# Kernel optimization log

Measured on AMD Instinct MI355X. Metric: run time of the kernel, lower is better.

The kernel has to match this reference:

```python
import jax, jax.numpy as jnp
import numpy as np
import math

B, S, HID = 2, 2048, 2048
NH, NKV, HD = 32, 8, 64
THETA = 10000.0
EPS = 1e-6
LAYER_IDX = 1
LAMBDA_INIT = 0.8 - 0.6 * math.exp(-0.3 * LAYER_IDX)
LAMBDA_STD = 0.1


def setup_inputs() -> dict:
    key = jax.random.key(0)
    ks = jax.random.split(key, 10)
    hidden_states = jax.random.normal(ks[0], (B, S, HID), jnp.float32)
    # RoPE cos/sin, llama convention: emb = cat(freqs, freqs)
    inv_freq = 1.0 / (THETA ** (np.arange(0, HD, 2, dtype=np.float32) / HD))
    freqs = np.outer(np.arange(S, dtype=np.float32), inv_freq)  # [S, HD/2]
    emb = np.concatenate([freqs, freqs], axis=-1)                # [S, HD]
    cos = jnp.broadcast_to(jnp.asarray(np.cos(emb), jnp.float32)[None], (B, S, HD))
    sin = jnp.broadcast_to(jnp.asarray(np.sin(emb), jnp.float32)[None], (B, S, HD))
    # additive causal mask [B,1,S,S]
    causal = jnp.triu(jnp.full((S, S), -1e9, dtype=jnp.float32), k=1)
    attention_mask = jnp.broadcast_to(causal[None, None], (B, 1, S, S))
    sc = 0.02
    wq = sc * jax.random.normal(ks[1], (NH * HD, HID), jnp.float32)
    wk = sc * jax.random.normal(ks[2], (NKV * HD, HID), jnp.float32)
    wv = sc * jax.random.normal(ks[3], (NKV * HD, HID), jnp.float32)
    wo = sc * jax.random.normal(ks[4], (HID, NH * HD), jnp.float32)
    lambda_q1 = LAMBDA_STD * jax.random.normal(ks[5], (HD,), jnp.float32)
    lambda_k1 = LAMBDA_STD * jax.random.normal(ks[6], (HD,), jnp.float32)
    lambda_q2 = LAMBDA_STD * jax.random.normal(ks[7], (HD,), jnp.float32)
    lambda_k2 = LAMBDA_STD * jax.random.normal(ks[8], (HD,), jnp.float32)
    return {"hidden_states": hidden_states, "cos": cos, "sin": sin,
            "attention_mask": attention_mask, "wq": wq, "wk": wk, "wv": wv,
            "wo": wo, "lambda_q1": lambda_q1, "lambda_k1": lambda_k1,
            "lambda_q2": lambda_q2, "lambda_k2": lambda_k2}


def _rotate_half(x):
    x1, x2 = jnp.split(x, 2, axis=-1)
    return jnp.concatenate([-x2, x1], axis=-1)


def reference(hidden_states, cos, sin, attention_mask, wq, wk, wv, wo,
              lambda_q1, lambda_k1, lambda_q2, lambda_k2):
    b, s, _ = hidden_states.shape
    # projections -> [b, h, s, d]
    q = jnp.einsum('bsh,oh->bso', hidden_states, wq).reshape(b, s, NH, HD).transpose(0, 2, 1, 3)
    k = jnp.einsum('bsh,oh->bso', hidden_states, wk).reshape(b, s, NKV, HD).transpose(0, 2, 1, 3)
    v = jnp.einsum('bsh,oh->bso', hidden_states, wv).reshape(b, s, NKV, HD).transpose(0, 2, 1, 3)
    # rotary
    c, sn = cos[:, None], sin[:, None]  # [b,1,s,d]
    q = q * c + _rotate_half(q) * sn
    k = k * c + _rotate_half(k) * sn
    # GQA repeat
    groups = NH // NKV
    k = jnp.repeat(k, groups, axis=1)
    v = jnp.repeat(v, groups, axis=1)
    # diff-attention value trick: pair head i with head i+NH/2 -> [b, NH, s, 2d]
    v = jnp.concatenate([v[:, :NH // 2], v[:, NH // 2:]], axis=-1)  # [b, NH/2, s, 2d]
    v = jnp.concatenate([v, v], axis=1)                              # [b, NH, s, 2d]
    # scores + causal mask, stable softmax in fp32
    aw = jnp.einsum('bhqd,bhkd->bhqk', q, k) / math.sqrt(HD)
    aw = aw + attention_mask
    aw = jax.nn.softmax(aw.astype(jnp.float32), axis=-1).astype(q.dtype)
    ao = jnp.einsum('bhqk,bhkd->bhqd', aw, v)  # [b, NH, s, 2d]
    lam1 = jnp.exp(jnp.sum((lambda_q1 * lambda_k1).astype(jnp.float32)))
    lam2 = jnp.exp(jnp.sum((lambda_q2 * lambda_k2).astype(jnp.float32)))
    lam = (lam1 - lam2).astype(q.dtype) + LAMBDA_INIT
    a1, a2 = ao[:, :NH // 2], ao[:, NH // 2:]
    out = a1 - lam * a2  # [b, NH/2, s, 2d]
    # RMSNorm over last dim (no affine)
    out = out * jax.lax.rsqrt(jnp.mean(out * out, axis=-1, keepdims=True) + EPS)
    out = (1.0 - LAMBDA_INIT) * out
    out = out.transpose(0, 2, 1, 3).reshape(b, s, NH * HD)
    return jnp.einsum('bso,ho->bsh', out, wo)
```

## Files before the change

### kernel.cpp

```cpp
#include <hip/hip_runtime.h>

typedef __attribute__((ext_vector_type(8))) short bhalf8;
typedef __attribute__((ext_vector_type(4))) float floatx4;

constexpr int B_ = 2, S_ = 2048, HID_ = 2048, NH_ = 32, NKV_ = 8, HD_ = 64;
constexpr float LAMBDA_INIT_F = 0.35550906759096924f;
constexpr float EPS_ = 1e-6f;
constexpr float QSCALE_ = 0.18033688011112042f;

#define DEVINL __device__ __forceinline__

DEVINL float bf2f(unsigned short u) {
    union { unsigned u; float f; } v; v.u = ((unsigned)u) << 16; return v.f;
}
DEVINL unsigned short f2bf(float f) {
    union { float f; unsigned u; } v; v.f = f;
    unsigned u = v.u;
    return (unsigned short)((u + 0x7fffu + ((u >> 16) & 1u)) >> 16);
}
DEVINL float fexp2(float x) {
#if __has_builtin(__builtin_amdgcn_exp2f)
    return __builtin_amdgcn_exp2f(x);
#else
    return exp2f(x);
#endif
}
DEVINL unsigned pk_bf16(float a, float b) {
#if __has_builtin(__builtin_amdgcn_cvt_pk_bf16_f32)
    typedef __bf16 bf16x2_t __attribute__((ext_vector_type(2)));
    bf16x2_t p = __builtin_amdgcn_cvt_pk_bf16_f32(a, b);
    unsigned r;
    __builtin_memcpy(&r, &p, 4);
    return r;
#else
    return (unsigned)f2bf(a) | ((unsigned)f2bf(b) << 16);
#endif
}
DEVINL void load_lds16(const unsigned short* g, unsigned short* l) {
    __builtin_amdgcn_global_load_lds(
        (const __attribute__((address_space(1))) unsigned int*)g,
        (__attribute__((address_space(3))) unsigned int*)l, 16, 0, 0);
}

__global__ __launch_bounds__(256)
void cvt_all(const float* __restrict__ hs, const float* __restrict__ wq,
             const float* __restrict__ wk, const float* __restrict__ wv,
             const float* __restrict__ wo, unsigned short* __restrict__ hs_bf,
             unsigned short* __restrict__ wcat, unsigned short* __restrict__ wo_bf) {
    const size_t i = (size_t)(blockIdx.x * 256 + threadIdx.x) * 4;
    const float* src;
    unsigned short* dst;
    size_t off;
    float scale = 1.f;
    if (i < 8388608) { src = hs; dst = hs_bf; off = 0; }
    else if (i < 12582912) { src = wq; dst = wcat; off = 8388608; scale = QSCALE_; }
    else if (i < 13631488) { src = wk; dst = wcat + 4194304; off = 12582912; }
    else if (i < 14680064) { src = wv; dst = wcat + 5242880; off = 13631488; }
    else { src = wo; dst = wo_bf; off = 14680064; }
    const size_t k = i - off;
    const float4 v = *(const float4*)(src + k);
    ushort4 o;
    o.x = f2bf(v.x * scale); o.y = f2bf(v.y * scale);
    o.z = f2bf(v.z * scale); o.w = f2bf(v.w * scale);
    *(ushort4*)(dst + k) = o;
}

__global__ void lam_kernel(const float* __restrict__ q1, const float* __restrict__ k1,
                           const float* __restrict__ q2, const float* __restrict__ k2,
                           float* __restrict__ lam) {
    const int l = threadIdx.x;
    float p1 = q1[l] * k1[l];
    float p2 = q2[l] * k2[l];
    #pragma unroll
    for (int off = 1; off < 64; off <<= 1) {
        p1 += __shfl_xor(p1, off, 64);
        p2 += __shfl_xor(p2, off, 64);
    }
    if (l == 0) *lam = expf(p1) - expf(p2) + LAMBDA_INIT_F;
}

__global__ __launch_bounds__(256)
void gemm_qkv(const unsigned short* __restrict__ A, const unsigned short* __restrict__ Bw,
              const float* __restrict__ cosb, const float* __restrict__ sinb,
              unsigned short* __restrict__ Qr, unsigned short* __restrict__ Kr,
              unsigned short* __restrict__ VT) {
    constexpr int K = 2048;
    union GS {
        struct { unsigned short A[2][128][32]; unsigned short B[2][128][32]; } d;
        unsigned short vt[128][130];
    };
    __shared__ __align__(16) GS gsm;
    const int t = threadIdx.x;
    const int w = t >> 6, lane = t & 63, quad = lane >> 4, lid = lane & 15;
    const int wr = (w >> 1) * 64, wc = (w & 1) * 64;
    const long bm = (long)blockIdx.x * 128, bn = (long)blockIdx.y * 128;

    floatx4 acc[4][4];
    #pragma unroll
    for (int i = 0; i < 4; i++)
        #pragma unroll
        for (int j = 0; j < 4; j++) acc[i][j] = (floatx4){0.f, 0.f, 0.f, 0.f};

    const int s0 = t, s1 = t + 256;
    const unsigned short* Ag0 = A + (bm + (s0 >> 2)) * (long)K + (s0 & 3) * 8;
    const unsigned short* Ag1 = A + (bm + (s1 >> 2)) * (long)K + (s1 & 3) * 8;
    const unsigned short* Bg0 = Bw + (bn + (s0 >> 2)) * (long)K + (s0 & 3) * 8;
    const unsigned short* Bg1 = Bw + (bn + (s1 >> 2)) * (long)K + (s1 & 3) * 8;
    const int l0 = s0 * 8, l1 = s1 * 8;

    load_lds16(Ag0, &gsm.d.A[0][0][0] + l0);
    load_lds16(Ag1, &gsm.d.A[0][0][0] + l1);
    load_lds16(Bg0, &gsm.d.B[0][0][0] + l0);
    load_lds16(Bg1, &gsm.d.B[0][0][0] + l1);
    __syncthreads();

    const int nk = K >> 5;
    for (int kt = 0; kt < nk; kt++) {
        const int cur = kt & 1, nxt = cur ^ 1;
        if (kt + 1 < nk) {
            const int off = (kt + 1) << 5;
            load_lds16(Ag0 + off, &gsm.d.A[nxt][0][0] + l0);
            load_lds16(Ag1 + off, &gsm.d.A[nxt][0][0] + l1);
            load_lds16(Bg0 + off, &gsm.d.B[nxt][0][0] + l0);
            load_lds16(Bg1 + off, &gsm.d.B[nxt][0][0] + l1);
        }
        bhalf8 af[4], bf[4];
        #pragma unroll
        for (int i = 0; i < 4; i++) af[i] = *(const bhalf8*)&gsm.d.A[cur][wr + i * 16 + lid][quad * 8];
        #pragma unroll
        for (int j = 0; j < 4; j++) bf[j] = *(const bhalf8*)&gsm.d.B[cur][wc + j * 16 + lid][quad * 8];
        #pragma unroll
        for (int i = 0; i < 4; i++)
            #pragma unroll
            for (int j = 0; j < 4; j++)
                acc[i][j] = __builtin_amdgcn_mfma_f32_16x16x32_bf16(af[i], bf[j], acc[i][j], 0, 0, 0);
        __syncthreads();
    }

    const int y = blockIdx.y;
    if (y < 20) {
        const bool isQ = (y < 16);
        #pragma unroll
        for (int i = 0; i < 4; i++) {
            #pragma unroll
            for (int r = 0; r < 4; r++) {
                const long row = bm + wr + i * 16 + quad * 4 + r;
                const int bb = (int)(row >> 11), s = (int)(row & 2047);
                const float* cp = cosb + (size_t)row * 64;
                const float* sp = sinb + (size_t)row * 64;
                #pragma unroll
                for (int jj = 0; jj < 4; jj++) {
                    const int col = (int)bn + wc + jj * 16 + lid;
                    const int d = col & 63;
                    const float x = acc[i][jj][r];
                    const float oth = acc[i][jj ^ 2][r];
                    const float rot = (jj < 2) ? -oth : oth;
                    const float yv = x * cp[d] + rot * sp[d];
                    if (isQ) {
                        const int h = col >> 6;
                        Qr[((size_t)(bb * NH_ + h) * S_ + s) * HD_ + d] = f2bf(yv);
                    } else {
                        const int h = (col - 2048) >> 6;
                        Kr[((size_t)(bb * NKV_ + h) * S_ + s) * HD_ + d] = f2bf(yv);
                    }
                }
            }
        }
    } else {
        #pragma unroll
        for (int i = 0; i < 4; i++)
            #pragma unroll
            for (int jj = 0; jj < 4; jj++)
                #pragma unroll
                for (int r = 0; r < 4; r++)
                    gsm.vt[wr + i * 16 + quad * 4 + r][wc + jj * 16 + lid] = f2bf(acc[i][jj][r]);
        __syncthreads();
        const int b0 = (int)(bm >> 11), sbase = (int)(bm & 2047);
        #pragma unroll 4
        for (int it = 0; it < 32; it++) {
            const int d = w + 4 * it;
            const int colg = (int)bn + d;
            const int h = (colg - 2560) >> 6;
            const int dl = colg & 63;
            const int sl = lane * 2;
            const unsigned v = (unsigned)gsm.vt[sl][d] | ((unsigned)gsm.vt[sl + 1][d] << 16);
            *(unsigned*)(VT + ((size_t)(b0 * NKV_ + h) * HD_ + dl) * S_ + sbase + sl) = v;
        }
    }
}

__global__ __launch_bounds__(256)
void gemm_bt(const unsigned short* __restrict__ A, const unsigned short* __restrict__ Bw,
             float* __restrict__ Cout, int M, int N, int K) {
    __shared__ __align__(16) unsigned short As[2][128][32];
    __shared__ __align__(16) unsigned short Bs[2][128][32];
    const int t = threadIdx.x;
    const int w = t >> 6, lane = t & 63, quad = lane >> 4, lid = lane & 15;
    const int wr = (w >> 1) * 64, wc = (w & 1) * 64;
    const long bm = (long)blockIdx.x * 128, bn = (long)blockIdx.y * 128;

    floatx4 acc[4][4];
    #pragma unroll
    for (int i = 0; i < 4; i++)
        #pragma unroll
        for (int j = 0; j < 4; j++) acc[i][j] = (floatx4){0.f, 0.f, 0.f, 0.f};

    const int s0 = t, s1 = t + 256;
    const unsigned short* Ag0 = A + (bm + (s0 >> 2)) * (long)K + (s0 & 3) * 8;
    const unsigned short* Ag1 = A + (bm + (s1 >> 2)) * (long)K + (s1 & 3) * 8;
    const unsigned short* Bg0 = Bw + (bn + (s0 >> 2)) * (long)K + (s0 & 3) * 8;
    const unsigned short* Bg1 = Bw + (bn + (s1 >> 2)) * (long)K + (s1 & 3) * 8;
    const int l0 = s0 * 8, l1 = s1 * 8;

    load_lds16(Ag0, &As[0][0][0] + l0);
    load_lds16(Ag1, &As[0][0][0] + l1);
    load_lds16(Bg0, &Bs[0][0][0] + l0);
    load_lds16(Bg1, &Bs[0][0][0] + l1);
    __syncthreads();

    const int nk = K >> 5;
    for (int kt = 0; kt < nk; kt++) {
        const int cur = kt & 1, nxt = cur ^ 1;
        if (kt + 1 < nk) {
            const int off = (kt + 1) << 5;
            load_lds16(Ag0 + off, &As[nxt][0][0] + l0);
            load_lds16(Ag1 + off, &As[nxt][0][0] + l1);
            load_lds16(Bg0 + off, &Bs[nxt][0][0] + l0);
            load_lds16(Bg1 + off, &Bs[nxt][0][0] + l1);
        }
        bhalf8 af[4], bf[4];
        #pragma unroll
        for (int i = 0; i < 4; i++) af[i] = *(const bhalf8*)&As[cur][wr + i * 16 + lid][quad * 8];
        #pragma unroll
        for (int j = 0; j < 4; j++) bf[j] = *(const bhalf8*)&Bs[cur][wc + j * 16 + lid][quad * 8];
        #pragma unroll
        for (int i = 0; i < 4; i++)
            #pragma unroll
            for (int j = 0; j < 4; j++)
                acc[i][j] = __builtin_amdgcn_mfma_f32_16x16x32_bf16(af[i], bf[j], acc[i][j], 0, 0, 0);
        __syncthreads();
    }

    #pragma unroll
    for (int i = 0; i < 4; i++) {
        #pragma unroll
        for (int j = 0; j < 4; j++) {
            const long row = bm + wr + i * 16 + quad * 4;
            const long col = bn + wc + j * 16 + lid;
            #pragma unroll
            for (int r = 0; r < 4; r++) Cout[(row + r) * N + col] = acc[i][j][r];
        }
    }
}

__global__ __launch_bounds__(512, 4)
void attn_diff(const unsigned short* __restrict__ Qr, const unsigned short* __restrict__ Kr,
               const unsigned short* __restrict__ VT, const float* __restrict__ lamp,
               unsigned short* __restrict__ attn) {
    union SM {
        struct {
            unsigned short Kt[2][64][72];
            unsigned short Vt[128][72];
            unsigned short Pt[8][16][72];
        } a;
        unsigned short Ot[2][64][136];
    };
    __shared__ __align__(16) SM sm;

    const int j = blockIdx.y, b = blockIdx.z;
    const int t = threadIdx.x;
    const int w = t >> 6, lane = t & 63, quad = lane >> 4, lid = lane & 15;
    const int st = w >> 2;
    const int rh = (w & 3) * 16;
    const int kv1 = j >> 2, kv2 = 4 + (j >> 2);
    const int qhead = j + st * 16;
    const float lam = *lamp;

    const int ss = t >> 8, kidx = t & 255;
    const int key_s = kidx >> 2, dh = (kidx & 3) * 16;
    const unsigned short* ksrc0 = Kr + (size_t)(b * NKV_ + (ss ? kv2 : kv1)) * S_ * HD_ +
                                  (size_t)key_s * HD_ + dh;
    const int d7 = t >> 2, vh = (t & 3) * 16;
    const unsigned short* vsrc0 = VT + ((size_t)(b * NKV_ + (d7 < 64 ? kv1 : kv2)) * HD_ +
                                        (d7 & 63)) * (size_t)S_ + vh;

    for (int half = 0; half < 2; half++) {
        const int qt = half ? (31 - (int)blockIdx.x) : (int)blockIdx.x;
        const int qb = qt * 64;

        const unsigned short* qbase =
            Qr + ((size_t)((b * NH_ + qhead) * S_) + qb + rh + lid) * HD_;
        const bhalf8 qa0 = *(const bhalf8*)(qbase + quad * 8);
        const bhalf8 qa1 = *(const bhalf8*)(qbase + 32 + quad * 8);

        floatx4 acc[8];
        #pragma unroll
        for (int c = 0; c < 8; c++) acc[c] = (floatx4){0.f, 0.f, 0.f, 0.f};
        float l_acc[4] = {0.f, 0.f, 0.f, 0.f};

        const int nkt = qt + 1;

        for (int kt = 0; kt < nkt; kt++) {
            const int k0 = kt * 64;
            const unsigned short* kp = ksrc0 + (size_t)k0 * HD_;
            const unsigned short* vp = vsrc0 + k0;
            int4 kr0 = *(const int4*)(kp);
            int4 kr1 = *(const int4*)(kp + 8);
            int4 vr0 = *(const int4*)(vp);
            int4 vr1 = *(const int4*)(vp + 8);
            __syncthreads();
            *(int4*)&sm.a.Kt[ss][key_s][dh] = kr0;
            *(int4*)&sm.a.Kt[ss][key_s][dh + 8] = kr1;
            *(int4*)&sm.a.Vt[d7][vh] = vr0;
            *(int4*)&sm.a.Vt[d7][vh + 8] = vr1;
            __syncthreads();

            const bool last = (kt == nkt - 1);
            const int nt_lim = last ? ((w & 3) + 1) : 4;

            floatx4 sc[4];
            #pragma unroll
            for (int nt = 0; nt < 4; nt++) {
                if (nt < nt_lim) {
                    const bhalf8 kb0 = *(const bhalf8*)&sm.a.Kt[st][nt * 16 + lid][quad * 8];
                    const bhalf8 kb1 = *(const bhalf8*)&sm.a.Kt[st][nt * 16 + lid][32 + quad * 8];
                    floatx4 z = (floatx4){0.f, 0.f, 0.f, 0.f};
                    z = __builtin_amdgcn_mfma_f32_16x16x32_bf16(qa0, kb0, z, 0, 0, 0);
                    z = __builtin_amdgcn_mfma_f32_16x16x32_bf16(qa1, kb1, z, 0, 0, 0);
                    sc[nt] = z;
                }
            }

            if (last) {
                #pragma unroll
                for (int nt = 0; nt < 4; nt++) {
                    const int keyg = k0 + nt * 16 + lid;
                    #pragma unroll
                    for (int r = 0; r < 4; r++) {
                        float p = 0.f;
                        if (nt < nt_lim) {
                            const int rowg = qb + rh + quad * 4 + r;
                            p = (keyg > rowg) ? 0.f : fexp2(sc[nt][r]);
                        }
                        sc[nt][r] = p;
                        l_acc[r] += p;
                    }
                }
            } else {
                #pragma unroll
                for (int nt = 0; nt < 4; nt++)
                    #pragma unroll
                    for (int r = 0; r < 4; r++) {
                        const float p = fexp2(sc[nt][r]);
                        sc[nt][r] = p;
                        l_acc[r] += p;
                    }
            }

            #pragma unroll
            for (int nt = 0; nt < 4; nt++) {
                #pragma unroll
                for (int r = 0; r < 4; r += 2) {
                    const unsigned pk = pk_bf16(sc[nt][r], sc[nt][r + 1]);
                    sm.a.Pt[w][quad * 4 + r][nt * 16 + lid] = (unsigned short)(pk & 0xffff);
                    sm.a.Pt[w][quad * 4 + r + 1][nt * 16 + lid] = (unsigned short)(pk >> 16);
                }
            }

            #pragma unroll
            for (int kk = 0; kk < 2; kk++) {
                if (nt_lim > kk * 2) {
                    const bhalf8 pa = *(const bhalf8*)&sm.a.Pt[w][lid][kk * 32 + quad * 8];
                    #pragma unroll
                    for (int c = 0; c < 8; c++) {
                        const bhalf8 vb = *(const bhalf8*)&sm.a.Vt[c * 16 + lid][kk * 32 + quad * 8];
                        acc[c] = __builtin_amdgcn_mfma_f32_16x16x32_bf16(pa, vb, acc[c], 0, 0, 0);
                    }
                }
            }
        }

        #pragma unroll
        for (int off = 1; off < 16; off <<= 1)
            #pragma unroll
            for (int r = 0; r < 4; r++) l_acc[r] += __shfl_xor(l_acc[r], off, 64);

        __syncthreads();
        #pragma unroll
        for (int r = 0; r < 4; r++) {
            const float rl = 1.0f / l_acc[r];
            #pragma unroll
            for (int c = 0; c < 8; c++)
                sm.Ot[st][rh + quad * 4 + r][c * 16 + lid] = f2bf(acc[c][r] * rl);
        }
        __syncthreads();

        const int row = t >> 3, m = t & 7;
        float vals[16];
        float ssum = 0.f;
        #pragma unroll
        for (int c = 0; c < 4; c++) {
            const unsigned long long u0 = *(const unsigned long long*)&sm.Ot[0][row][m * 4 + 32 * c];
            const unsigned long long u1 = *(const unsigned long long*)&sm.Ot[1][row][m * 4 + 32 * c];
            #pragma unroll
            for (int i = 0; i < 4; i++) {
                const float x = bf2f((unsigned short)(u0 >> (16 * i))) -
                                lam * bf2f((unsigned short)(u1 >> (16 * i)));
                vals[c * 4 + i] = x;
                ssum += x * x;
            }
        }
        ssum += __shfl_xor(ssum, 1, 64);
        ssum += __shfl_xor(ssum, 2, 64);
        ssum += __shfl_xor(ssum, 4, 64);
        const float scale = (1.f - LAMBDA_INIT_F) * rsqrtf(ssum * (1.f / 128.f) + EPS_);
        unsigned short* dst = attn + (size_t)(b * S_ + qb + row) * (NH_ * HD_) + j * 128 + m * 4;
        #pragma unroll
        for (int c = 0; c < 4; c++) {
            unsigned short ob[4];
            #pragma unroll
            for (int i = 0; i < 4; i++) ob[i] = f2bf(vals[c * 4 + i] * scale);
            *(unsigned long long*)(dst + 32 * c) = *(const unsigned long long*)ob;
        }
        __syncthreads();
    }
}

extern "C" void kernel_launch(void* const* d_in, const int* in_sizes, int n_in,
                              void* d_out, int out_size, void* d_ws, size_t ws_size,
                              hipStream_t stream) {
    const float* hs   = (const float*)d_in[0];
    const float* cosb = (const float*)d_in[1];
    const float* sinb = (const float*)d_in[2];
    const float* wq   = (const float*)d_in[4];
    const float* wk   = (const float*)d_in[5];
    const float* wv   = (const float*)d_in[6];
    const float* wo   = (const float*)d_in[7];
    const float* lq1  = (const float*)d_in[8];
    const float* lk1  = (const float*)d_in[9];
    const float* lq2  = (const float*)d_in[10];
    const float* lk2  = (const float*)d_in[11];

    unsigned short* p = (unsigned short*)d_ws;
    unsigned short* hs_bf = p;  p += (size_t)4096 * 2048;
    unsigned short* wcat  = p;  p += (size_t)3072 * 2048;
    unsigned short* wo_bf = p;  p += (size_t)2048 * 2048;
    unsigned short* Qr    = p;  p += (size_t)B_ * NH_ * S_ * HD_;
    unsigned short* Kr    = p;  p += (size_t)B_ * NKV_ * S_ * HD_;
    unsigned short* VT    = p;  p += (size_t)B_ * NKV_ * S_ * HD_;
    unsigned short* attnb = p;  p += (size_t)4096 * 2048;
    float* lam = (float*)p;

    cvt_all<<<18432, 256, 0, stream>>>(hs, wq, wk, wv, wo, hs_bf, wcat, wo_bf);
    lam_kernel<<<1, 64, 0, stream>>>(lq1, lk1, lq2, lk2, lam);
    gemm_qkv<<<dim3(32, 24), 256, 0, stream>>>(hs_bf, wcat, cosb, sinb, Qr, Kr, VT);
    attn_diff<<<dim3(16, 16, 2), 512, 0, stream>>>(Qr, Kr, VT, lam, attnb);
    gemm_bt<<<dim3(32, 16), 256, 0, stream>>>(attnb, wo_bf, (float*)d_out, 4096, 2048, 2048);
}
```

Measured before the change: 358.4 us.

## Prefetch next K/V tile into registers and raise wave priority around MFMA

The attention loop now issues the global loads for the next K/V tile right after storing the current tile to shared memory, so their latency overlaps with the QK and PV compute instead of stalling at the loop top. The __syncthreads calls become explicit waitcnt plus s_barrier with sched_barrier fences, and s_setprio brackets the MFMA sections so matrix work gets issue priority. The output staging buffer padding also shrinks from 136 to 132. The prefetch holds extra live registers, which may pressure occupancy under the 512x4 launch bounds, and the new padding may change LDS bank conflicts in the output staging.

```diff
diff --git a/kernel.cpp b/kernel.cpp
--- a/kernel.cpp
+++ b/kernel.cpp
@@ -263,7 +263,7 @@
             unsigned short Vt[128][72];
             unsigned short Pt[8][16][72];
         } a;
-        unsigned short Ot[2][64][136];
+        unsigned short Ot[2][64][132];
     };
     __shared__ __align__(16) SM sm;
 
@@ -300,25 +300,36 @@
 
         const int nkt = qt + 1;
 
+        int4 kr0 = *(const int4*)(ksrc0);
+        int4 kr1 = *(const int4*)(ksrc0 + 8);
+        int4 vr0 = *(const int4*)(vsrc0);
+        int4 vr1 = *(const int4*)(vsrc0 + 8);
+
         for (int kt = 0; kt < nkt; kt++) {
-            const int k0 = kt * 64;
-            const unsigned short* kp = ksrc0 + (size_t)k0 * HD_;
-            const unsigned short* vp = vsrc0 + k0;
-            int4 kr0 = *(const int4*)(kp);
-            int4 kr1 = *(const int4*)(kp + 8);
-            int4 vr0 = *(const int4*)(vp);
-            int4 vr1 = *(const int4*)(vp + 8);
-            __syncthreads();
+            asm volatile("s_waitcnt vmcnt(0)" ::: "memory");
+            __builtin_amdgcn_s_barrier();
+            __builtin_amdgcn_sched_barrier(0);
             *(int4*)&sm.a.Kt[ss][key_s][dh] = kr0;
             *(int4*)&sm.a.Kt[ss][key_s][dh + 8] = kr1;
             *(int4*)&sm.a.Vt[d7][vh] = vr0;
             *(int4*)&sm.a.Vt[d7][vh + 8] = vr1;
-            __syncthreads();
+            if (kt + 1 < nkt) {
+                const unsigned short* kp = ksrc0 + (size_t)(kt + 1) * 64 * HD_;
+                const unsigned short* vp = vsrc0 + (kt + 1) * 64;
+                kr0 = *(const int4*)(kp);
+                kr1 = *(const int4*)(kp + 8);
+                vr0 = *(const int4*)(vp);
+                vr1 = *(const int4*)(vp + 8);
+            }
+            asm volatile("s_waitcnt lgkmcnt(0)" ::: "memory");
+            __builtin_amdgcn_s_barrier();
+            __builtin_amdgcn_sched_barrier(0);
 
             const bool last = (kt == nkt - 1);
             const int nt_lim = last ? ((w & 3) + 1) : 4;
 
             floatx4 sc[4];
+            __builtin_amdgcn_s_setprio(1);
             #pragma unroll
             for (int nt = 0; nt < 4; nt++) {
                 if (nt < nt_lim) {
@@ -330,11 +341,12 @@
                     sc[nt] = z;
                 }
             }
+            __builtin_amdgcn_s_setprio(0);
 
             if (last) {
                 #pragma unroll
                 for (int nt = 0; nt < 4; nt++) {
-                    const int keyg = k0 + nt * 16 + lid;
+                    const int keyg = kt * 64 + nt * 16 + lid;
                     #pragma unroll
                     for (int r = 0; r < 4; r++) {
                         float p = 0.f;
@@ -367,6 +379,7 @@
                 }
             }
 
+            __builtin_amdgcn_s_setprio(1);
             #pragma unroll
             for (int kk = 0; kk < 2; kk++) {
                 if (nt_lim > kk * 2) {
@@ -378,6 +391,7 @@
                     }
                 }
             }
+            __builtin_amdgcn_s_setprio(0);
         }
 
         #pragma unroll
```

Result: no change. 351.9 us (-1.8%).
